# Kernel optimization log

Measured on AMD Instinct MI355X. Metric: run time of the kernel, lower is better.

## Reference

```python
import jax, jax.numpy as jnp
import numpy as np

B, QLEN, DM = 32, 1, 1024
H, DK = 16, 64
TCACHE = 4096


def setup_inputs() -> dict:
    key = jax.random.key(0)
    ks = jax.random.split(key, 11)
    s = 1.0 / np.sqrt(DM)
    return {
        "q": jax.random.normal(ks[0], (B, QLEN, DM), jnp.float32),
        "key_pre": jax.random.normal(ks[1], (B, H, TCACHE, DK), jnp.float32),
        "value_pre": jax.random.normal(ks[2], (B, H, TCACHE, DK), jnp.float32),
        "wq": jax.random.normal(ks[3], (DM, DM), jnp.float32) * s,
        "bq": jax.random.normal(ks[4], (DM,), jnp.float32) * 0.01,
        "wk": jax.random.normal(ks[5], (DM, DM), jnp.float32) * s,
        "bk": jax.random.normal(ks[6], (DM,), jnp.float32) * 0.01,
        "wv": jax.random.normal(ks[7], (DM, DM), jnp.float32) * s,
        "bv": jax.random.normal(ks[8], (DM,), jnp.float32) * 0.01,
        "wo": jax.random.normal(ks[9], (DM, DM), jnp.float32) * s,
        "bo": jax.random.normal(ks[10], (DM,), jnp.float32) * 0.01,
    }


def reference(q, key_pre, value_pre, wq, bq, wk, bk, wv, bv, wo, bo):
    b, t, _ = q.shape
    # QKV projections (nn.Linear: x @ W.T + b), reshape to [B, H, T, DK]
    def proj(w, bias):
        return (q @ w.T + bias).reshape(b, t, H, DK).transpose(0, 2, 1, 3)
    query = proj(wq, bq)                               # [B,H,1,DK]
    k_new = proj(wk, bk)
    v_new = proj(wv, bv)
    # KV-cache append (torch.cat along time dim)
    k = jnp.concatenate([key_pre, k_new], axis=2)      # [B,H,Tc+1,DK]
    v = jnp.concatenate([value_pre, v_new], axis=2)
    # scaled dot-product attention (mask=None, dropout inactive/eval)
    scores = jnp.einsum("bhqd,bhkd->bhqk", query, k) / jnp.sqrt(jnp.float32(DK))
    attn = jax.nn.softmax(scores, axis=-1)
    x = jnp.einsum("bhqk,bhkd->bhqd", attn, v)         # [B,H,1,DK]
    x = x.transpose(0, 2, 1, 3).reshape(b, t, H * DK)
    out = x @ wo.T + bo                                # [B,1,DM]
    return out
```

## Files before the change

kernel.cpp:

```cpp
#include <hip/hip_runtime.h>
#include <math.h>

#define B   32
#define H   16
#define DK  64
#define DM  1024
#define TC  4096
#define NS  8
#define DSL 8
#define LOG2E 1.44269504088896340736f
#define SCALE 0.125f

__global__ __launch_bounds__(256) void proj_partial(
    const float* __restrict__ in,
    const float* __restrict__ w0,
    const float* __restrict__ w1,
    const float* __restrict__ w2,
    float* __restrict__ part)
{
    const int jt = blockIdx.x;
    const int ds = blockIdx.y;
    const int m  = blockIdx.z;
    const float* __restrict__ w = (m == 0) ? w0 : (m == 1) ? w1 : w2;

    __shared__ float qs[32 * 132];
    const float4* in4 = (const float4*)in;
    float4* qs4 = (float4*)qs;
    const int tid = threadIdx.x;

    #pragma unroll
    for (int k = 0; k < 4; k++) {
        int g   = tid + k * 256;
        int b   = g >> 5;
        int dd4 = g & 31;
        qs4[b * 33 + dd4] = in4[b * 256 + ds * 32 + dd4];
    }
    __syncthreads();

    const int wave  = tid >> 6;
    const int lane  = tid & 63;
    const int jhalf = lane >> 5;
    const int b     = lane & 31;
    const float4* w4 = (const float4*)w;

    #pragma unroll
    for (int p = 0; p < 8; p++) {
        int j = jt * 64 + wave * 16 + p * 2 + jhalf;
        float acc = 0.f;
        #pragma unroll
        for (int it = 0; it < 32; it++) {
            float4 wv = w4[j * 256 + ds * 32 + it];
            float4 qv = qs4[b * 33 + it];
            acc += wv.x * qv.x + wv.y * qv.y + wv.z * qv.z + wv.w * qv.w;
        }
        part[((m * DSL + ds) * DM + j) * 32 + b] = acc;
    }
}

__global__ __launch_bounds__(256) void reduce_part(
    const float* __restrict__ part,
    const float* __restrict__ b0,
    const float* __restrict__ b1,
    const float* __restrict__ b2,
    float* __restrict__ out)
{
    const int gid = blockIdx.x * 256 + threadIdx.x;
    const int m = gid >> 15;
    const int r = gid & 32767;
    const int j = r >> 5;
    const int b = r & 31;
    float s = 0.f;
    #pragma unroll
    for (int ds = 0; ds < DSL; ds++)
        s += part[(m * DSL + ds) * (DM * 32) + r];
    const float* __restrict__ bias = (m == 0) ? b0 : (m == 1) ? b1 : b2;
    out[m * (B * DM) + b * DM + j] = s + bias[j];
}

__global__ __launch_bounds__(256) void attn_part_kernel(
    const float* __restrict__ qh,
    const float* __restrict__ Kc,
    const float* __restrict__ Vc,
    float* __restrict__ part_O,
    float* __restrict__ part_ml)
{
    const int split = blockIdx.x;
    const int h = blockIdx.y;
    const int b = blockIdx.z;
    const int bh = b * H + h;
    const int t0 = split * (TC / NS);

    __shared__ float sp[512];
    __shared__ float so[16 * 64];
    __shared__ float red[8];

    const int tid = threadIdx.x;
    const int r = tid >> 4;
    const int c = tid & 15;

    const float4* q4p = (const float4*)(qh + b * DM + h * DK);
    const float4 q4 = q4p[c];

    const float4* K4 = (const float4*)(Kc + (size_t)bh * TC * DK);
    const float4* V4 = (const float4*)(Vc + (size_t)bh * TC * DK);
    const float sc = SCALE * LOG2E;

    #pragma unroll 4
    for (int it = 0; it < 32; it++) {
        int t = t0 + it * 16 + r;
        float4 k4 = K4[t * 16 + c];
        float d = q4.x * k4.x + q4.y * k4.y + q4.z * k4.z + q4.w * k4.w;
        d += __shfl_xor(d, 1);
        d += __shfl_xor(d, 2);
        d += __shfl_xor(d, 4);
        d += __shfl_xor(d, 8);
        if (c == 0) sp[it * 16 + r] = d * sc;
    }
    __syncthreads();

    float v0 = sp[tid], v1 = sp[tid + 256];
    float mx = fmaxf(v0, v1);
    #pragma unroll
    for (int o = 32; o; o >>= 1) mx = fmaxf(mx, __shfl_xor(mx, o));
    if ((tid & 63) == 0) red[tid >> 6] = mx;
    __syncthreads();
    mx = fmaxf(fmaxf(red[0], red[1]), fmaxf(red[2], red[3]));

    float p0 = exp2f(v0 - mx);
    float p1 = exp2f(v1 - mx);
    sp[tid] = p0;
    sp[tid + 256] = p1;
    float sm = p0 + p1;
    #pragma unroll
    for (int o = 32; o; o >>= 1) sm += __shfl_xor(sm, o);
    if ((tid & 63) == 0) red[4 + (tid >> 6)] = sm;
    __syncthreads();
    const float l = red[4] + red[5] + red[6] + red[7];

    float4 acc = make_float4(0.f, 0.f, 0.f, 0.f);
    #pragma unroll 4
    for (int it = 0; it < 32; it++) {
        int t = t0 + it * 16 + r;
        float4 vv = V4[t * 16 + c];
        float pp = sp[it * 16 + r];
        acc.x += pp * vv.x;
        acc.y += pp * vv.y;
        acc.z += pp * vv.z;
        acc.w += pp * vv.w;
    }
    float4* so4 = (float4*)so;
    so4[r * 16 + c] = acc;
    __syncthreads();

    if (tid < 64) {
        float od = 0.f;
        #pragma unroll
        for (int rr = 0; rr < 16; rr++) od += so[rr * 64 + tid];
        part_O[(bh * NS + split) * 64 + tid] = od;
    }
    if (tid == 0) {
        part_ml[(bh * NS + split) * 2 + 0] = mx;
        part_ml[(bh * NS + split) * 2 + 1] = l;
    }
}

__global__ __launch_bounds__(64) void combine_kernel(
    const float* __restrict__ qh,
    const float* __restrict__ kn,
    const float* __restrict__ vn,
    const float* __restrict__ part_O,
    const float* __restrict__ part_ml,
    float* __restrict__ x)
{
    const int bh = blockIdx.x;
    const int b = bh >> 4;
    const int h = bh & 15;
    const int d = threadIdx.x;
    const int off = b * DM + h * DK + d;

    const float qv = qh[off];
    const float kv = kn[off];
    const float vv = vn[off];

    float s = qv * kv;
    s += __shfl_xor(s, 1);
    s += __shfl_xor(s, 2);
    s += __shfl_xor(s, 4);
    s += __shfl_xor(s, 8);
    s += __shfl_xor(s, 16);
    s += __shfl_xor(s, 32);
    const float snew = s * (SCALE * LOG2E);

    float mvals[NS], lvals[NS];
    float M = snew;
    #pragma unroll
    for (int i = 0; i < NS; i++) {
        mvals[i] = part_ml[(bh * NS + i) * 2 + 0];
        lvals[i] = part_ml[(bh * NS + i) * 2 + 1];
        M = fmaxf(M, mvals[i]);
    }
    const float wn = exp2f(snew - M);
    float L = wn;
    float od = vv * wn;
    #pragma unroll
    for (int i = 0; i < NS; i++) {
        float wgt = exp2f(mvals[i] - M);
        L += lvals[i] * wgt;
        od += part_O[(bh * NS + i) * 64 + d] * wgt;
    }
    x[bh * 64 + d] = od / L;
}

extern "C" void kernel_launch(void* const* d_in, const int* in_sizes, int n_in,
                              void* d_out, int out_size, void* d_ws, size_t ws_size,
                              hipStream_t stream) {
    const float* q  = (const float*)d_in[0];
    const float* Kc = (const float*)d_in[1];
    const float* Vc = (const float*)d_in[2];
    const float* wq = (const float*)d_in[3];
    const float* bq = (const float*)d_in[4];
    const float* wk = (const float*)d_in[5];
    const float* bk = (const float*)d_in[6];
    const float* wv = (const float*)d_in[7];
    const float* bv = (const float*)d_in[8];
    const float* wo = (const float*)d_in[9];
    const float* bo = (const float*)d_in[10];
    float* out = (float*)d_out;
    float* ws = (float*)d_ws;

    float* part   = ws;
    float* qkv    = ws + 786432;
    float* partO  = ws + 786432 + 98304;
    float* partml = ws + 786432 + 98304 + 262144;
    float* x      = ws + 786432 + 98304 + 262144 + 8192;
    float* qh = qkv;
    float* kn = qkv + 32768;
    float* vn = qkv + 65536;

    proj_partial<<<dim3(16, DSL, 3), 256, 0, stream>>>(q, wq, wk, wv, part);
    reduce_part<<<dim3(3 * 32768 / 256), 256, 0, stream>>>(part, bq, bk, bv, qkv);

    attn_part_kernel<<<dim3(NS, H, B), 256, 0, stream>>>(qh, Kc, Vc, partO, partml);

    combine_kernel<<<dim3(B * H), 64, 0, stream>>>(qh, kn, vn, partO, partml, x);

    proj_partial<<<dim3(16, DSL, 1), 256, 0, stream>>>(x, wo, wo, wo, part);
    reduce_part<<<dim3(32768 / 256), 256, 0, stream>>>(part, bo, bo, bo, out);
}
```

Baseline: 1.072 ms.

## Fuse QK and PV passes into single-pass online softmax per wave

Measured after the change: 1.067 ms. Within noise of the previous version (-0.4%).

```diff
diff --git a/kernel.cpp b/kernel.cpp
--- a/kernel.cpp
+++ b/kernel.cpp
@@ -90,77 +90,87 @@
     const int bh = b * H + h;
     const int t0 = split * (TC / NS);
 
-    __shared__ float sp[512];
-    __shared__ float so[16 * 64];
-    __shared__ float red[8];
-
-    const int tid = threadIdx.x;
-    const int r = tid >> 4;
-    const int c = tid & 15;
-
-    const float4* q4p = (const float4*)(qh + b * DM + h * DK);
-    const float4 q4 = q4p[c];
-
+    __shared__ float so[4 * 64];
+    __shared__ float sml[8];
+
+    const int tid  = threadIdx.x;
+    const int wave = tid >> 6;
+    const int lane = tid & 63;
+    const int r = lane >> 4;
+    const int c = lane & 15;
+
+    const float4 q4 = ((const float4*)(qh + b * DM + h * DK))[c];
     const float4* K4 = (const float4*)(Kc + (size_t)bh * TC * DK);
     const float4* V4 = (const float4*)(Vc + (size_t)bh * TC * DK);
     const float sc = SCALE * LOG2E;
 
+    float m = -1e30f;
+    float l = 0.f;
+    float4 acc = make_float4(0.f, 0.f, 0.f, 0.f);
+
+    const int base = t0 + wave * 128;
+
     #pragma unroll 4
     for (int it = 0; it < 32; it++) {
-        int t = t0 + it * 16 + r;
+        int t = base + it * 4 + r;
         float4 k4 = K4[t * 16 + c];
+        float4 v4 = V4[t * 16 + c];
         float d = q4.x * k4.x + q4.y * k4.y + q4.z * k4.z + q4.w * k4.w;
         d += __shfl_xor(d, 1);
         d += __shfl_xor(d, 2);
         d += __shfl_xor(d, 4);
         d += __shfl_xor(d, 8);
-        if (c == 0) sp[it * 16 + r] = d * sc;
+        float s = d * sc;
+        float mo = m;
+        m = fmaxf(m, s);
+        float f = exp2f(mo - m);
+        float p = exp2f(s - m);
+        l = l * f + p;
+        acc.x = acc.x * f + p * v4.x;
+        acc.y = acc.y * f + p * v4.y;
+        acc.z = acc.z * f + p * v4.z;
+        acc.w = acc.w * f + p * v4.w;
+    }
+
+    #pragma unroll
+    for (int off = 16; off <= 32; off <<= 1) {
+        float mo = __shfl_xor(m, off);
+        float lo = __shfl_xor(l, off);
+        float ax = __shfl_xor(acc.x, off);
+        float ay = __shfl_xor(acc.y, off);
+        float az = __shfl_xor(acc.z, off);
+        float aw = __shfl_xor(acc.w, off);
+        float M  = fmaxf(m, mo);
+        float fs = exp2f(m - M);
+        float fo = exp2f(mo - M);
+        m = M;
+        l = l * fs + lo * fo;
+        acc.x = acc.x * fs + ax * fo;
+        acc.y = acc.y * fs + ay * fo;
+        acc.z = acc.z * fs + az * fo;
+        acc.w = acc.w * fs + aw * fo;
+    }
+
+    if (lane < 16) {
+        ((float4*)&so[wave * 64])[c] = acc;
+        if (c == 0) { sml[wave * 2] = m; sml[wave * 2 + 1] = l; }
     }
     __syncthreads();
 
-    float v0 = sp[tid], v1 = sp[tid + 256];
-    float mx = fmaxf(v0, v1);
-    #pragma unroll
-    for (int o = 32; o; o >>= 1) mx = fmaxf(mx, __shfl_xor(mx, o));
-    if ((tid & 63) == 0) red[tid >> 6] = mx;
-    __syncthreads();
-    mx = fmaxf(fmaxf(red[0], red[1]), fmaxf(red[2], red[3]));
-
-    float p0 = exp2f(v0 - mx);
-    float p1 = exp2f(v1 - mx);
-    sp[tid] = p0;
-    sp[tid + 256] = p1;
-    float sm = p0 + p1;
-    #pragma unroll
-    for (int o = 32; o; o >>= 1) sm += __shfl_xor(sm, o);
-    if ((tid & 63) == 0) red[4 + (tid >> 6)] = sm;
-    __syncthreads();
-    const float l = red[4] + red[5] + red[6] + red[7];
-
-    float4 acc = make_float4(0.f, 0.f, 0.f, 0.f);
-    #pragma unroll 4
-    for (int it = 0; it < 32; it++) {
-        int t = t0 + it * 16 + r;
-        float4 vv = V4[t * 16 + c];
-        float pp = sp[it * 16 + r];
-        acc.x += pp * vv.x;
-        acc.y += pp * vv.y;
-        acc.z += pp * vv.z;
-        acc.w += pp * vv.w;
-    }
-    float4* so4 = (float4*)so;
-    so4[r * 16 + c] = acc;
-    __syncthreads();
-
     if (tid < 64) {
-        float od = 0.f;
+        const float M = fmaxf(fmaxf(sml[0], sml[2]), fmaxf(sml[4], sml[6]));
+        float L = 0.f, od = 0.f;
         #pragma unroll
-        for (int rr = 0; rr < 16; rr++) od += so[rr * 64 + tid];
+        for (int w = 0; w < 4; w++) {
+            float f = exp2f(sml[w * 2] - M);
+            L  += sml[w * 2 + 1] * f;
+            od += so[w * 64 + tid] * f;
+        }
         part_O[(bh * NS + split) * 64 + tid] = od;
-    }
-    if (tid == 0) {
-        part_ml[(bh * NS + split) * 2 + 0] = mx;
-        part_ml[(bh * NS + split) * 2 + 1] = l;
+        if (tid == 0) {
+            part_ml[(bh * NS + split) * 2 + 0] = M;
+            part_ml[(bh * NS + split) * 2 + 1] = L;
+        }
     }
 }
 
```
